# Optimization experiments

Measured on AMD Instinct MI355X. Metric: run time of the kernel, lower is better.

The kernel has to match this reference:

```python
import jax, jax.numpy as jnp
import numpy as np

B, LP, LQ, CL = 64, 64, 64, 8
VW, VC = 30002, 5002
WD, CD, CH, H, P = 300, 64, 64, 128, 20
EPS = 1e-6


def _norm(x, eps=EPS):
    # torch: sqrt(clamp(sum(x^2, -1), min=eps))
    return jnp.sqrt(jnp.maximum(jnp.sum(x * x, -1), eps))


def lstm_scan(x, Wih, Whh, b):
    # x: [N, T, D] -> outputs [N, T, Hh]; PyTorch gate order i,f,g,o
    N = x.shape[0]
    Hh = Whh.shape[1]
    xW = jnp.einsum('ntd,gd->ntg', x, Wih) + b  # precompute input projection
    def step(carry, xt):
        h, c = carry
        g = xt + h @ Whh.T
        i, f, gg, o = jnp.split(g, 4, axis=-1)
        c = jax.nn.sigmoid(f) * c + jax.nn.sigmoid(i) * jnp.tanh(gg)
        h = jax.nn.sigmoid(o) * jnp.tanh(c)
        return (h, c), h
    init = (jnp.zeros((N, Hh), x.dtype), jnp.zeros((N, Hh), x.dtype))
    _, hs = jax.lax.scan(step, init, jnp.swapaxes(xW, 0, 1))
    return jnp.swapaxes(hs, 0, 1)


def bilstm(x, Wf, Uf, bf, Wb, Ub, bb):
    fw = lstm_scan(x, Wf, Uf, bf)
    bw = jnp.flip(lstm_scan(jnp.flip(x, axis=1), Wb, Ub, bb), axis=1)
    return fw, bw


def mpm(p_fw, p_bw, q_fw, q_bw, ws):
    # ws: [8, P, H]
    def full(h1, h2, w):
        h1w = h1[:, :, None, :] * w              # [B,L,P,H]
        h2w = h2[:, -1, None, :] * w             # [B,P,H]
        num = jnp.einsum('blpd,bpd->blp', h1w, h2w)
        return num / _norm(h1w) / _norm(h2w)[:, None, :]
    def cos_matrix(x1, x2):
        num = jnp.einsum('bid,bjd->bij', x1, x2)
        return num / _norm(x1)[:, :, None] / _norm(x2)[:, None, :]
    def attentive(h1, h2, cm, w):
        h1w = h1[:, :, None, :] * w
        att = jnp.einsum('bij,bjd->bid', cm, h2) / (cm.sum(-1) + EPS)[..., None]
        attw = att[:, :, None, :] * w
        num = jnp.sum(h1w * attw, -1)
        return num / _norm(h1w) / _norm(attw)
    def max_attentive(h1, h2, cm, w):
        idx = jnp.argmax(cm, axis=-1)                           # [B,Lp]
        mv = jnp.take_along_axis(h2, idx[:, :, None], axis=1)   # [B,Lp,H]
        h1w = h1[:, :, None, :] * w
        mvw = mv[:, :, None, :] * w
        num = jnp.sum(h1w * mvw, -1)
        return num / _norm(h1w) / _norm(mvw)
    def max_pool(h1, h2, w):
        h1w = h1[:, :, None, :] * w
        h2w = h2[:, :, None, :] * w
        num = jnp.einsum('bipd,bjpd->bijp', h1w, h2w)           # [B,Lp,Lq,P]
        cos = num / _norm(h1w)[:, :, None, :] / _norm(h2w)[:, None, :, :]
        return cos.max(axis=2)
    cm_fw = cos_matrix(p_fw, q_fw)
    cm_bw = cos_matrix(p_bw, q_bw)
    return jnp.concatenate([
        full(p_fw, q_fw, ws[0]), full(p_bw, q_bw, ws[1]),
        attentive(p_fw, q_fw, cm_fw, ws[2]), attentive(p_bw, q_bw, cm_bw, ws[3]),
        max_attentive(p_fw, q_fw, cm_fw, ws[4]), max_attentive(p_bw, q_bw, cm_bw, ws[5]),
        max_pool(p_fw, q_fw, ws[6]), max_pool(p_bw, q_bw, ws[7])], axis=-1)


def setup_inputs():
    key = jax.random.key(0)
    ks = jax.random.split(key, 24)
    rn = lambda k, s, sc=0.1: jax.random.normal(k, s, dtype=jnp.float32) * sc
    def lstm_w(k, din, h):
        k1, k2 = jax.random.split(k)
        return rn(k1, (4 * h, din)), rn(k2, (4 * h, h)), jnp.zeros((4 * h,), jnp.float32)
    cWih, cWhh, cb = lstm_w(ks[4], CD, CH)
    xWf, xUf, xbf = lstm_w(ks[5], CH + WD, H)
    xWb, xUb, xbb = lstm_w(ks[6], CH + WD, H)
    aWf, aUf, abf = lstm_w(ks[7], 8 * P, H)
    aWb, aUb, abb = lstm_w(ks[8], 8 * P, H)
    return {
        'contentA_idxs': jax.random.randint(ks[0], (B, LP), 0, VW),
        'contentB_idxs': jax.random.randint(ks[1], (B, LQ), 0, VW),
        'contentA_char_idxs': jax.random.randint(ks[2], (B, LP, CL), 0, VC),
        'contentB_char_idxs': jax.random.randint(ks[3], (B, LQ, CL), 0, VC),
        'word_emb': rn(ks[9], (VW, WD), 1.0),
        'char_emb': rn(ks[10], (VC, CD), 1.0),
        'char_Wih': cWih, 'char_Whh': cWhh, 'char_b': cb,
        'ctx_Wih_f': xWf, 'ctx_Whh_f': xUf, 'ctx_b_f': xbf,
        'ctx_Wih_b': xWb, 'ctx_Whh_b': xUb, 'ctx_b_b': xbb,
        'agg_Wih_f': aWf, 'agg_Whh_f': aUf, 'agg_b_f': abf,
        'agg_Wih_b': aWb, 'agg_Whh_b': aUb, 'agg_b_b': abb,
        'mpm_w': rn(ks[11], (8, P, H), 1.0),
        'fc1_W': rn(ks[12], (2 * H, 4 * H), 0.005), 'fc1_b': jnp.zeros((2 * H,), jnp.float32),
        'fc2_W': rn(ks[13], (2, 2 * H), 0.005), 'fc2_b': jnp.zeros((2,), jnp.float32),
    }


def reference(contentA_idxs, contentB_idxs, contentA_char_idxs, contentB_char_idxs,
              word_emb, char_emb, char_Wih, char_Whh, char_b,
              ctx_Wih_f, ctx_Whh_f, ctx_b_f, ctx_Wih_b, ctx_Whh_b, ctx_b_b,
              agg_Wih_f, agg_Whh_f, agg_b_f, agg_Wih_b, agg_Whh_b, agg_b_b,
              mpm_w, fc1_W, fc1_b, fc2_W, fc2_b):
    def encode(word_idx, char_idx):
        w = word_emb[word_idx]                                   # [B,L,WD]
        L = word_idx.shape[1]
        c = char_emb[char_idx].reshape(B * L, CL, CD)
        ch = lstm_scan(c, char_Wih, char_Whh, char_b)[:, -1, :]  # last hidden
        x = jnp.concatenate([w, ch.reshape(B, L, CH)], axis=-1)
        return bilstm(x, ctx_Wih_f, ctx_Whh_f, ctx_b_f, ctx_Wih_b, ctx_Whh_b, ctx_b_b)
    p_fw, p_bw = encode(contentA_idxs, contentA_char_idxs)
    q_fw, q_bw = encode(contentB_idxs, contentB_char_idxs)
    mp = mpm(p_fw, p_bw, q_fw, q_bw, mpm_w)  # [B,LP,8P]
    mq = mpm(q_fw, q_bw, p_fw, p_bw, mpm_w)  # [B,LQ,8P]
    ap_fw, ap_bw = bilstm(mp, agg_Wih_f, agg_Whh_f, agg_b_f, agg_Wih_b, agg_Whh_b, agg_b_b)
    aq_fw, aq_bw = bilstm(mq, agg_Wih_f, agg_Whh_f, agg_b_f, agg_Wih_b, agg_Whh_b, agg_b_b)
    x = jnp.concatenate([ap_fw[:, -1], ap_bw[:, 0], aq_fw[:, -1], aq_bw[:, 0]], axis=-1)
    x = jnp.tanh(x @ fc1_W.T + fc1_b)
    return x @ fc2_W.T + fc2_b  # [B,2] logits
```

## Files before the change

kernel.cpp:

```cpp
#include <hip/hip_runtime.h>

#define EPS 1e-6f

typedef __attribute__((ext_vector_type(8))) short short8;
typedef __attribute__((ext_vector_type(8))) _Float16 half8;
typedef __attribute__((ext_vector_type(4))) float floatx4;

struct ScanArgs {
    const float* xw[4];
    const float* whh[4];
    float* out[4];
    int flipOut[4];
    int writeAll;
    int outStride;
};

struct MfArgs {
    const unsigned short* X;
    const unsigned short* W[4];
    const float* bias[4];
    float* out[4];
    int flip[4];
    int rowBase[4];
    int Kaug;
};

__device__ __forceinline__ float fsig(float x) { return 1.0f / (1.0f + __expf(-x)); }
__device__ __forceinline__ float tanh_fast(float x) {
    float e = __expf(2.f * x);
    return 1.f - 2.f / (e + 1.f);
}
__device__ __forceinline__ unsigned short f2bf(float x) {
    unsigned u = __float_as_uint(x);
    return (unsigned short)((u + 0x7fffu + ((u >> 16) & 1u)) >> 16);
}
__device__ __forceinline__ void split8_bf(const float* p, short8& hi, short8& lo) {
    #pragma unroll
    for (int e = 0; e < 8; ++e) {
        unsigned short h = f2bf(p[e]);
        float hf = __uint_as_float((unsigned)h << 16);
        hi[e] = (short)h;
        lo[e] = (short)f2bf(p[e] - hf);
    }
}
__device__ __forceinline__ void split8_f16(const float* p, half8& hi, half8& lo) {
    #pragma unroll
    for (int e = 0; e < 8; ++e) {
        _Float16 h = (_Float16)p[e];
        hi[e] = h;
        lo[e] = (_Float16)(p[e] - (float)h);
    }
}

__global__ void k_embed_word(const int* __restrict__ idxA, const int* __restrict__ idxB,
                             const float* __restrict__ emb,
                             float* __restrict__ xA, float* __restrict__ xB) {
    int row = blockIdx.x;
    const int* idx = (row < 4096) ? idxA : idxB;
    float* xout = (row < 4096) ? xA : xB;
    int r = row & 4095;
    size_t e = (size_t)idx[r];
    const float* src = emb + e * 300;
    float* dst = xout + (size_t)r * 364;
    for (int d = threadIdx.x; d < 300; d += blockDim.x) dst[d] = src[d];
}

__global__ void k_conv(const float* __restrict__ src, unsigned short* __restrict__ dst,
                       int K, int Ksec, int isW) {
    int row = blockIdx.x;
    const float* s = src + (size_t)row * K;
    unsigned short* d = dst + (size_t)row * (3 * Ksec);
    int o1 = (isW ? 2 : 1) * Ksec;
    int o2 = (isW ? 1 : 2) * Ksec;
    for (int k = threadIdx.x; k < Ksec; k += blockDim.x) {
        float x = (k < K) ? s[k] : 0.f;
        unsigned short hr = f2bf(x);
        float hif = __uint_as_float((unsigned)hr << 16);
        unsigned short lr2 = f2bf(x - hif);
        d[k]      = hr;
        d[o1 + k] = lr2;
        d[o2 + k] = hr;
    }
}

__global__ __launch_bounds__(256, 1)
void k_char_mfma(const int* __restrict__ cidxA, const int* __restrict__ cidxB,
                 const float* __restrict__ emb,
                 const unsigned short* __restrict__ WihA, const unsigned short* __restrict__ WhhA,
                 const float* __restrict__ bias,
                 float* __restrict__ xA, float* __restrict__ xB) {
    __shared__ __align__(16) float xs[32][68];
    __shared__ __align__(16) float hs[32][68];
    int tid = threadIdx.x;
    int w = tid >> 6, l = tid & 63, lr = l & 15, lc = l >> 4;
    int j = w * 16 + lr;
    short8 wih[4][6], whh[4][6];
    #pragma unroll
    for (int g = 0; g < 4; ++g)
        #pragma unroll
        for (int kt = 0; kt < 6; ++kt) {
            wih[g][kt] = *(const short8*)&WihA[(size_t)(g*64 + j)*192 + kt*32 + lc*8];
            whh[g][kt] = *(const short8*)&WhhA[(size_t)(g*64 + j)*192 + kt*32 + lc*8];
        }
    float bg[4];
    #pragma unroll
    for (int g = 0; g < 4; ++g) bg[g] = bias[g*64 + j];
    int seq0 = blockIdx.x * 32;
    for (int m = tid; m < 32*68; m += 256) (&hs[0][0])[m] = 0.f;
    float cst[2][4] = {};
    float hlast[2][4];
    __syncthreads();
    for (int t = 0; t < 8; ++t) {
        {
            int s = tid >> 3, ch = tid & 7;
            int sq = seq0 + s;
            const int* ci = (sq < 4096) ? cidxA : cidxB;
            int e = ci[(sq & 4095)*8 + t];
            float4 v0 = *(const float4*)&emb[(size_t)e*64 + ch*8];
            float4 v1 = *(const float4*)&emb[(size_t)e*64 + ch*8 + 4];
            *(float4*)&xs[s][ch*8] = v0;
            *(float4*)&xs[s][ch*8 + 4] = v1;
        }
        short8 hhi[2][2], hlo[2][2];
        if (t > 0) {
            #pragma unroll
            for (int mt = 0; mt < 2; ++mt)
                #pragma unroll
                for (int kt = 0; kt < 2; ++kt) {
                    float tmp[8];
                    *(float4*)&tmp[0] = *(const float4*)&hs[mt*16 + lr][kt*32 + lc*8];
                    *(float4*)&tmp[4] = *(const float4*)&hs[mt*16 + lr][kt*32 + lc*8 + 4];
                    split8_bf(tmp, hhi[mt][kt], hlo[mt][kt]);
                }
        }
        __syncthreads();
        short8 xhi[2][2], xlo[2][2];
        #pragma unroll
        for (int mt = 0; mt < 2; ++mt)
            #pragma unroll
            for (int kt = 0; kt < 2; ++kt) {
                float tmp[8];
                *(float4*)&tmp[0] = *(const float4*)&xs[mt*16 + lr][kt*32 + lc*8];
                *(float4*)&tmp[4] = *(const float4*)&xs[mt*16 + lr][kt*32 + lc*8 + 4];
                split8_bf(tmp, xhi[mt][kt], xlo[mt][kt]);
            }
        #pragma unroll
        for (int mt = 0; mt < 2; ++mt)
            #pragma unroll
            for (int g = 0; g < 4; ++g) {
                floatx4 a = {bg[g], bg[g], bg[g], bg[g]};
                a = __builtin_amdgcn_mfma_f32_16x16x32_bf16(xhi[mt][0], wih[g][0], a, 0, 0, 0);
                a = __builtin_amdgcn_mfma_f32_16x16x32_bf16(xhi[mt][1], wih[g][1], a, 0, 0, 0);
                a = __builtin_amdgcn_mfma_f32_16x16x32_bf16(xlo[mt][0], wih[g][2], a, 0, 0, 0);
                a = __builtin_amdgcn_mfma_f32_16x16x32_bf16(xlo[mt][1], wih[g][3], a, 0, 0, 0);
                a = __builtin_amdgcn_mfma_f32_16x16x32_bf16(xhi[mt][0], wih[g][4], a, 0, 0, 0);
                a = __builtin_amdgcn_mfma_f32_16x16x32_bf16(xhi[mt][1], wih[g][5], a, 0, 0, 0);
                if (t > 0) {
                    a = __builtin_amdgcn_mfma_f32_16x16x32_bf16(hhi[mt][0], whh[g][0], a, 0, 0, 0);
                    a = __builtin_amdgcn_mfma_f32_16x16x32_bf16(hhi[mt][1], whh[g][1], a, 0, 0, 0);
                    a = __builtin_amdgcn_mfma_f32_16x16x32_bf16(hlo[mt][0], whh[g][2], a, 0, 0, 0);
                    a = __builtin_amdgcn_mfma_f32_16x16x32_bf16(hlo[mt][1], whh[g][3], a, 0, 0, 0);
                    a = __builtin_amdgcn_mfma_f32_16x16x32_bf16(hhi[mt][0], whh[g][4], a, 0, 0, 0);
                    a = __builtin_amdgcn_mfma_f32_16x16x32_bf16(hhi[mt][1], whh[g][5], a, 0, 0, 0);
                }
                if (g == 0) { hlast[mt][0] = a[0]; hlast[mt][1] = a[1]; hlast[mt][2] = a[2]; hlast[mt][3] = a[3]; }
                else if (g == 1) {
                    #pragma unroll
                    for (int i = 0; i < 4; ++i) cst[mt][i] = fsig(a[i]) * cst[mt][i];
                } else if (g == 2) {
                    #pragma unroll
                    for (int i = 0; i < 4; ++i) cst[mt][i] += fsig(hlast[mt][i]) * tanh_fast(a[i]);
                } else {
                    #pragma unroll
                    for (int i = 0; i < 4; ++i) {
                        float h = fsig(a[i]) * tanh_fast(cst[mt][i]);
                        hlast[mt][i] = h;
                        hs[mt*16 + lc*4 + i][j] = h;
                    }
                }
            }
        __syncthreads();
    }
    #pragma unroll
    for (int mt = 0; mt < 2; ++mt)
        #pragma unroll
        for (int i = 0; i < 4; ++i) {
            int s = mt*16 + lc*4 + i;
            int sq = seq0 + s;
            float* xout = (sq < 4096) ? xA : xB;
            xout[(size_t)(sq & 4095)*364 + 300 + j] = hlast[mt][i];
        }
}

__global__ __launch_bounds__(256, 2)
void k_xw_mfma(MfArgs a) {
    int scan = blockIdx.z;
    const unsigned short* X = a.X;
    const unsigned short* W = a.W[scan];
    const float* bias = a.bias[scan];
    float* out = a.out[scan];
    int flip = a.flip[scan];
    int rowBase = a.rowBase[scan];
    int Kaug = a.Kaug;
    int m0 = blockIdx.x * 128;
    int n0 = blockIdx.y * 128;
    __shared__ __align__(16) unsigned short As[128][40];
    __shared__ __align__(16) unsigned short Bs[128][40];
    int tid = threadIdx.x;
    int wv = tid >> 6, lane = tid & 63;
    int lr = lane & 15, lc = lane >> 4;

    floatx4 acc[2][8];
    #pragma unroll
    for (int f = 0; f < 2; ++f)
        #pragma unroll
        for (int g = 0; g < 8; ++g)
            acc[f][g] = (floatx4){0.f, 0.f, 0.f, 0.f};

    int r0 = m0 + (tid >> 2);
    int r1 = r0 + 64;
    int sr0 = rowBase + (flip ? ((r0 & ~63) | (63 - (r0 & 63))) : r0);
    int sr1 = rowBase + (flip ? ((r1 & ~63) | (63 - (r1 & 63))) : r1);
    size_t asrc0 = (size_t)sr0 * Kaug + (tid & 3) * 8;
    size_t asrc1 = (size_t)sr1 * Kaug + (tid & 3) * 8;
    size_t bsrc0 = (size_t)(n0 + (tid >> 2)) * Kaug + (tid & 3) * 8;
    size_t bsrc1 = (size_t)(n0 + (tid >> 2) + 64) * Kaug + (tid & 3) * 8;
    int swrow = tid >> 2, swcol = (tid & 3) * 8;

    for (int k0 = 0; k0 < Kaug; k0 += 32) {
        short8 a0 = *(const short8*)(X + asrc0 + k0);
        short8 a1 = *(const short8*)(X + asrc1 + k0);
        short8 b0 = *(const short8*)(W + bsrc0 + k0);
        short8 b1 = *(const short8*)(W + bsrc1 + k0);
        __syncthreads();
        *(short8*)&As[swrow][swcol]      = a0;
        *(short8*)&As[swrow + 64][swcol] = a1;
        *(short8*)&Bs[swrow][swcol]      = b0;
        *(short8*)&Bs[swrow + 64][swcol] = b1;
        __syncthreads();
        short8 af0 = *(const short8*)&As[wv*32 + lr][lc*8];
        short8 af1 = *(const short8*)&As[wv*32 + 16 + lr][lc*8];
        #pragma unroll
        for (int g = 0; g < 8; ++g) {
            short8 bf = *(const short8*)&Bs[g*16 + lr][lc*8];
            acc[0][g] = __builtin_amdgcn_mfma_f32_16x16x32_bf16(af0, bf, acc[0][g], 0, 0, 0);
            acc[1][g] = __builtin_amdgcn_mfma_f32_16x16x32_bf16(af1, bf, acc[1][g], 0, 0, 0);
        }
    }

    #pragma unroll
    for (int f = 0; f < 2; ++f) {
        int row = m0 + wv*32 + f*16 + lc*4;
        #pragma unroll
        for (int g = 0; g < 8; ++g) {
            int col = n0 + g*16 + lr;
            float bv = bias[col];
            #pragma unroll
            for (int i = 0; i < 4; ++i)
                out[(size_t)(row + i)*512 + col] = acc[f][g][i] + bv;
        }
    }
}

__global__ __launch_bounds__(512, 2)
void k_lstm_scan(ScanArgs a) {
    int b = blockIdx.x;
    int scan = blockIdx.y;
    int tid = threadIdx.x;
    __shared__ __align__(16) float h_lds[128];
    __shared__ float g_lds[512];
    const float* W = a.whh[scan];
    float w[128];
    #pragma unroll
    for (int k4 = 0; k4 < 32; ++k4) {
        float4 v = *(const float4*)&W[(size_t)tid*128 + k4*4];
        w[k4*4+0]=v.x; w[k4*4+1]=v.y; w[k4*4+2]=v.z; w[k4*4+3]=v.w;
    }
    const float* xw = a.xw[scan] + (size_t)b*64*512;
    float* outp = a.out[scan];
    int flip = a.flipOut[scan];
    int wAll = a.writeAll;
    float c = 0.f;
    if (tid < 128) h_lds[tid] = 0.f;
    __syncthreads();
    for (int t = 0; t < 64; ++t) {
        float a0 = xw[t*512 + tid], a1 = 0.f, a2 = 0.f, a3 = 0.f;
        #pragma unroll
        for (int k16 = 0; k16 < 8; ++k16) {
            float4 h0 = *(const float4*)&h_lds[k16*16+0];
            float4 h1 = *(const float4*)&h_lds[k16*16+4];
            float4 h2 = *(const float4*)&h_lds[k16*16+8];
            float4 h3 = *(const float4*)&h_lds[k16*16+12];
            a0 += w[k16*16+ 0]*h0.x + w[k16*16+ 1]*h0.y + w[k16*16+ 2]*h0.z + w[k16*16+ 3]*h0.w;
            a1 += w[k16*16+ 4]*h1.x + w[k16*16+ 5]*h1.y + w[k16*16+ 6]*h1.z + w[k16*16+ 7]*h1.w;
            a2 += w[k16*16+ 8]*h2.x + w[k16*16+ 9]*h2.y + w[k16*16+10]*h2.z + w[k16*16+11]*h2.w;
            a3 += w[k16*16+12]*h3.x + w[k16*16+13]*h3.y + w[k16*16+14]*h3.z + w[k16*16+15]*h3.w;
        }
        g_lds[tid] = (a0+a1)+(a2+a3);
        __syncthreads();
        if (tid < 128) {
            float gi = g_lds[tid], gf = g_lds[128+tid], gg = g_lds[256+tid], go = g_lds[384+tid];
            c = fsig(gf)*c + fsig(gi)*tanhf(gg);
            float h = fsig(go)*tanhf(c);
            h_lds[tid] = h;
            if (wAll) {
                int tout = flip ? (63 - t) : t;
                outp[((size_t)b*64 + tout)*128 + tid] = h;
            }
        }
        __syncthreads();
    }
    if (!wAll && tid < 128)
        outp[(size_t)b * a.outStride + tid] = h_lds[tid];
}

__global__ __launch_bounds__(256, 1)
void k_cos_matrix(const float* __restrict__ pfw, const float* __restrict__ pbw,
                  const float* __restrict__ qfw, const float* __restrict__ qbw,
                  float* __restrict__ cmf, float* __restrict__ cmb) {
    int b = blockIdx.x, dir = blockIdx.y;
    const float* h1 = (dir ? pbw : pfw) + (size_t)b*8192;
    const float* h2 = (dir ? qbw : qfw) + (size_t)b*8192;
    float* cm = (dir ? cmb : cmf) + (size_t)b*4096;
    __shared__ __align__(16) float A[64][132];
    __shared__ __align__(16) float Bt[64][132];
    __shared__ float n1[64], n2[64];
    int tid = threadIdx.x;
    for (int m = tid; m < 8192; m += 256) {
        int r = m >> 7, d = m & 127;
        A[r][d] = h1[m];
        Bt[r][d] = h2[m];
    }
    __syncthreads();
    if (tid < 128) {
        const float* row = (tid < 64) ? &A[tid][0] : &Bt[tid-64][0];
        float s = 0.f;
        #pragma unroll
        for (int k4 = 0; k4 < 32; ++k4) {
            float4 v = *(const float4*)&row[k4*4];
            s += v.x*v.x + v.y*v.y + v.z*v.z + v.w*v.w;
        }
        float nv = sqrtf(fmaxf(s, EPS));
        if (tid < 64) n1[tid] = nv; else n2[tid-64] = nv;
    }
    __syncthreads();
    int tx = tid & 15, ty = tid >> 4;
    float acc[4][4] = {};
    #pragma unroll
    for (int k4 = 0; k4 < 32; ++k4) {
        float4 av[4], bv[4];
        #pragma unroll
        for (int i = 0; i < 4; ++i) av[i] = *(const float4*)&A[ty + i*16][k4*4];
        #pragma unroll
        for (int j = 0; j < 4; ++j) bv[j] = *(const float4*)&Bt[tx + j*16][k4*4];
        #pragma unroll
        for (int i = 0; i < 4; ++i)
            #pragma unroll
            for (int j = 0; j < 4; ++j)
                acc[i][j] += av[i].x*bv[j].x + av[i].y*bv[j].y + av[i].z*bv[j].z + av[i].w*bv[j].w;
    }
    #pragma unroll
    for (int i = 0; i < 4; ++i) {
        int r = ty + i*16;
        #pragma unroll
        for (int j = 0; j < 4; ++j) {
            int c2 = tx + j*16;
            cm[r*64 + c2] = acc[i][j] / (n1[r]*n2[c2]);
        }
    }
}

__global__ __launch_bounds__(512, 2)
void k_full_att(const float* __restrict__ pfw, const float* __restrict__ pbw,
                const float* __restrict__ qfw, const float* __restrict__ qbw,
                const float* __restrict__ cmf, const float* __restrict__ cmb,
                const float* __restrict__ mpmw,
                float* __restrict__ mp, float* __restrict__ mq) {
    int b = blockIdx.x, dir = blockIdx.y, which = blockIdx.z;
    const float* pd = (dir ? pbw : pfw) + (size_t)b*8192;
    const float* qd = (dir ? qbw : qfw) + (size_t)b*8192;
    const float* h1g = which ? qd : pd;
    const float* h2g = which ? pd : qd;
    const float* cmsrc = (dir ? cmb : cmf) + (size_t)b*4096;
    float* outb = which ? mq : mp;
    __shared__ __align__(16) float h2s[64][132];
    __shared__ float cms[64][68];
    __shared__ __align__(16) float wl[3*20*128];
    int tid = threadIdx.x;
    for (int m = tid; m < 8192; m += 512) {
        int r = m >> 7, d = m & 127;
        h2s[r][d] = h2g[m];
    }
    for (int m = tid; m < 4096; m += 512) {
        int l = m >> 6, j = m & 63;
        cms[l][j] = which ? cmsrc[j*64 + l] : cmsrc[m];
    }
    for (int m = tid; m < 2560; m += 512) {
        wl[m]        = mpmw[(size_t)(0+dir)*2560 + m];
        wl[2560 + m] = mpmw[(size_t)(2+dir)*2560 + m];
        wl[5120 + m] = mpmw[(size_t)(4+dir)*2560 + m];
    }
    __syncthreads();
    int l = tid >> 3, r = tid & 7;
    int d0 = r * 16;
    float h1d[16];
    #pragma unroll
    for (int q4 = 0; q4 < 4; ++q4) {
        float4 v = *(const float4*)&h1g[l*128 + d0 + q4*4];
        h1d[q4*4+0]=v.x; h1d[q4*4+1]=v.y; h1d[q4*4+2]=v.z; h1d[q4*4+3]=v.w;
    }
    float rsum = 0.f, bv = -3.4e38f; int bj = 64;
    for (int jj = 0; jj < 8; ++jj) {
        int j = r*8 + jj;
        float cv = cms[l][j];
        rsum += cv;
        if (cv > bv) { bv = cv; bj = j; }
    }
    #pragma unroll
    for (int m = 1; m < 8; m <<= 1) rsum += __shfl_xor(rsum, m, 8);
    #pragma unroll
    for (int m = 1; m < 8; m <<= 1) {
        float ov = __shfl_xor(bv, m, 8);
        int oj = __shfl_xor(bj, m, 8);
        if (ov > bv || (ov == bv && oj < bj)) { bv = ov; bj = oj; }
    }
    float att[16];
    #pragma unroll
    for (int dd = 0; dd < 16; ++dd) att[dd] = 0.f;
    for (int j = 0; j < 64; ++j) {
        float cv = cms[l][j];
        #pragma unroll
        for (int q4 = 0; q4 < 4; ++q4) {
            float4 hv = *(const float4*)&h2s[j][d0 + q4*4];
            att[q4*4+0] += cv*hv.x; att[q4*4+1] += cv*hv.y;
            att[q4*4+2] += cv*hv.z; att[q4*4+3] += cv*hv.w;
        }
    }
    float rinv = 1.f / (rsum + EPS);
    #pragma unroll
    for (int dd = 0; dd < 16; ++dd) att[dd] *= rinv;
    float mvd[16], h2l[16];
    #pragma unroll
    for (int q4 = 0; q4 < 4; ++q4) {
        float4 v = *(const float4*)&h2s[bj][d0 + q4*4];
        mvd[q4*4+0]=v.x; mvd[q4*4+1]=v.y; mvd[q4*4+2]=v.z; mvd[q4*4+3]=v.w;
        float4 u = *(const float4*)&h2s[63][d0 + q4*4];
        h2l[q4*4+0]=u.x; h2l[q4*4+1]=u.y; h2l[q4*4+2]=u.z; h2l[q4*4+3]=u.w;
    }
    size_t outrow = ((size_t)b*64 + l)*160;
    for (int pp = 0; pp < 20; ++pp) {
        const float* wf = &wl[pp*128 + d0];
        const float* wa = &wl[2560 + pp*128 + d0];
        const float* wm = &wl[5120 + pp*128 + d0];
        float fn=0,f1=0,f2=0, an=0,a1=0,a2=0, mn=0,m1=0,m2=0;
        #pragma unroll
        for (int dd = 0; dd < 16; ++dd) {
            float wfv = wf[dd], wav = wa[dd], wmv = wm[dd];
            float x1 = h1d[dd]*wfv, x2 = h2l[dd]*wfv;
            fn += x1*x2; f1 += x1*x1; f2 += x2*x2;
            float y1 = h1d[dd]*wav, y2 = att[dd]*wav;
            an += y1*y2; a1 += y1*y1; a2 += y2*y2;
            float z1 = h1d[dd]*wmv, z2 = mvd[dd]*wmv;
            mn += z1*z2; m1 += z1*z1; m2 += z2*z2;
        }
        #pragma unroll
        for (int m = 1; m < 8; m <<= 1) {
            fn += __shfl_xor(fn,m,8); f1 += __shfl_xor(f1,m,8); f2 += __shfl_xor(f2,m,8);
            an += __shfl_xor(an,m,8); a1 += __shfl_xor(a1,m,8); a2 += __shfl_xor(a2,m,8);
            mn += __shfl_xor(mn,m,8); m1 += __shfl_xor(m1,m,8); m2 += __shfl_xor(m2,m,8);
        }
        if (r == 0) {
            outb[outrow + (0+dir)*20 + pp] = fn / sqrtf(fmaxf(f1,EPS)) / sqrtf(fmaxf(f2,EPS));
            outb[outrow + (2+dir)*20 + pp] = an / sqrtf(fmaxf(a1,EPS)) / sqrtf(fmaxf(a2,EPS));
            outb[outrow + (4+dir)*20 + pp] = mn / sqrtf(fmaxf(m1,EPS)) / sqrtf(fmaxf(m2,EPS));
        }
    }
}

__global__ __launch_bounds__(256, 1)
void k_maxpool_mfma(const float* __restrict__ pfw, const float* __restrict__ pbw,
                    const float* __restrict__ qfw, const float* __restrict__ qbw,
                    const float* __restrict__ mpmw,
                    float* __restrict__ mp, float* __restrict__ mq) {
    int b = blockIdx.x, dir = blockIdx.y, pph = blockIdx.z;
    const float* h1 = (dir ? pbw : pfw) + (size_t)b*8192;
    const float* h2 = (dir ? qbw : qfw) + (size_t)b*8192;
    __shared__ __align__(16) float h1s[64][132];
    __shared__ __align__(16) float h2s[64][132];
    __shared__ __align__(16) float w2s[32][132];
    __shared__ float n1s[64][25], n2s[64][25];
    __shared__ float cpart[4][68];
    int tid = threadIdx.x;
    int w = tid >> 6, l = tid & 63, lr = l & 15, lc = l >> 4;
    for (int m = tid; m < 8192; m += 256) {
        int r = m >> 7, d = m & 127;
        h1s[r][d] = h1[m];
        h2s[r][d] = h2[m];
    }
    for (int m = tid; m < 32*128; m += 256) {
        int r = m >> 7, d = m & 127;
        float v = (r < 20) ? mpmw[(size_t)((6+dir)*20 + r)*128 + d] : 0.f;
        w2s[r][d] = v * v;
    }
    __syncthreads();
    float a1[32], b1[32];
    #pragma unroll
    for (int kt = 0; kt < 4; ++kt) {
        *(float4*)&a1[kt*8]     = *(const float4*)&h1s[w*16 + lr][kt*32 + lc*8];
        *(float4*)&a1[kt*8 + 4] = *(const float4*)&h1s[w*16 + lr][kt*32 + lc*8 + 4];
        *(float4*)&b1[kt*8]     = *(const float4*)&h2s[w*16 + lr][kt*32 + lc*8];
        *(float4*)&b1[kt*8 + 4] = *(const float4*)&h2s[w*16 + lr][kt*32 + lc*8 + 4];
    }
    half8 Bh[4][4], Bl[4][4];
    #pragma unroll
    for (int nt = 0; nt < 4; ++nt)
        #pragma unroll
        for (int kt = 0; kt < 4; ++kt) {
            float tmp[8];
            *(float4*)&tmp[0] = *(const float4*)&h2s[nt*16 + lr][kt*32 + lc*8];
            *(float4*)&tmp[4] = *(const float4*)&h2s[nt*16 + lr][kt*32 + lc*8 + 4];
            split8_f16(tmp, Bh[nt][kt], Bl[nt][kt]);
        }
    {
        float sq[32];
        half8 s1h[4], s1l[4], s2h[4], s2l[4];
        #pragma unroll
        for (int kt = 0; kt < 4; ++kt) {
            #pragma unroll
            for (int e = 0; e < 8; ++e) sq[kt*8+e] = a1[kt*8+e]*a1[kt*8+e];
            split8_f16(&sq[kt*8], s1h[kt], s1l[kt]);
        }
        #pragma unroll
        for (int kt = 0; kt < 4; ++kt) {
            #pragma unroll
            for (int e = 0; e < 8; ++e) sq[kt*8+e] = b1[kt*8+e]*b1[kt*8+e];
            split8_f16(&sq[kt*8], s2h[kt], s2l[kt]);
        }
        half8 w2h[2][4], w2l[2][4];
        #pragma unroll
        for (int nt2 = 0; nt2 < 2; ++nt2)
            #pragma unroll
            for (int kt = 0; kt < 4; ++kt) {
                float tmp[8];
                *(float4*)&tmp[0] = *(const float4*)&w2s[nt2*16 + lr][kt*32 + lc*8];
                *(float4*)&tmp[4] = *(const float4*)&w2s[nt2*16 + lr][kt*32 + lc*8 + 4];
                split8_f16(tmp, w2h[nt2][kt], w2l[nt2][kt]);
            }
        #pragma unroll
        for (int nt2 = 0; nt2 < 2; ++nt2) {
            floatx4 na1 = {0.f,0.f,0.f,0.f}, na2 = {0.f,0.f,0.f,0.f};
            #pragma unroll
            for (int kt = 0; kt < 4; ++kt) {
                na1 = __builtin_amdgcn_mfma_f32_16x16x32_f16(s1h[kt], w2h[nt2][kt], na1, 0, 0, 0);
                na2 = __builtin_amdgcn_mfma_f32_16x16x32_f16(s2h[kt], w2h[nt2][kt], na2, 0, 0, 0);
            }
            #pragma unroll
            for (int kt = 0; kt < 4; ++kt) {
                na1 = __builtin_amdgcn_mfma_f32_16x16x32_f16(s1l[kt], w2h[nt2][kt], na1, 0, 0, 0);
                na2 = __builtin_amdgcn_mfma_f32_16x16x32_f16(s2l[kt], w2h[nt2][kt], na2, 0, 0, 0);
            }
            #pragma unroll
            for (int kt = 0; kt < 4; ++kt) {
                na1 = __builtin_amdgcn_mfma_f32_16x16x32_f16(s1h[kt], w2l[nt2][kt], na1, 0, 0, 0);
                na2 = __builtin_amdgcn_mfma_f32_16x16x32_f16(s2h[kt], w2l[nt2][kt], na2, 0, 0, 0);
            }
            #pragma unroll
            for (int i = 0; i < 4; ++i) {
                int row = w*16 + lc*4 + i;
                int c2 = nt2*16 + lr;
                if (c2 < 20) {
                    n1s[row][c2] = sqrtf(fmaxf(na1[i], EPS));
                    n2s[row][c2] = sqrtf(fmaxf(na2[i], EPS));
                }
            }
        }
    }
    __syncthreads();
    for (int pi = 0; pi < 10; ++pi) {
        int pp = pph*10 + pi;
        int col = (6+dir)*20 + pp;
        half8 ah[4], al[4];
        #pragma unroll
        for (int kt = 0; kt < 4; ++kt) {
            float wv[8], aw[8];
            *(float4*)&wv[0] = *(const float4*)&w2s[pp][kt*32 + lc*8];
            *(float4*)&wv[4] = *(const float4*)&w2s[pp][kt*32 + lc*8 + 4];
            #pragma unroll
            for (int e = 0; e < 8; ++e) aw[e] = a1[kt*8+e]*wv[e];
            split8_f16(aw, ah[kt], al[kt]);
        }
        float n1v[4];
        #pragma unroll
        for (int i = 0; i < 4; ++i) n1v[i] = n1s[w*16 + lc*4 + i][pp];
        float rmax[4] = {-3.4e38f, -3.4e38f, -3.4e38f, -3.4e38f};
        float cmx[4];
        #pragma unroll
        for (int nt = 0; nt < 4; ++nt) {
            floatx4 acc = {0.f,0.f,0.f,0.f};
            #pragma unroll
            for (int kt = 0; kt < 4; ++kt)
                acc = __builtin_amdgcn_mfma_f32_16x16x32_f16(ah[kt], Bh[nt][kt], acc, 0, 0, 0);
            #pragma unroll
            for (int kt = 0; kt < 4; ++kt)
                acc = __builtin_amdgcn_mfma_f32_16x16x32_f16(al[kt], Bh[nt][kt], acc, 0, 0, 0);
            #pragma unroll
            for (int kt = 0; kt < 4; ++kt)
                acc = __builtin_amdgcn_mfma_f32_16x16x32_f16(ah[kt], Bl[nt][kt], acc, 0, 0, 0);
            float n2v = n2s[nt*16 + lr][pp];
            float cm_ = -3.4e38f;
            #pragma unroll
            for (int i = 0; i < 4; ++i) {
                float cv = acc[i] / (n1v[i] * n2v);
                rmax[i] = fmaxf(rmax[i], cv);
                cm_ = fmaxf(cm_, cv);
            }
            cmx[nt] = cm_;
        }
        #pragma unroll
        for (int msk = 1; msk < 16; msk <<= 1)
            #pragma unroll
            for (int i = 0; i < 4; ++i) rmax[i] = fmaxf(rmax[i], __shfl_xor(rmax[i], msk));
        if (lr == 0) {
            #pragma unroll
            for (int i = 0; i < 4; ++i)
                mp[((size_t)b*64 + w*16 + lc*4 + i)*160 + col] = rmax[i];
        }
        #pragma unroll
        for (int msk = 16; msk < 64; msk <<= 1)
            #pragma unroll
            for (int nt = 0; nt < 4; ++nt) cmx[nt] = fmaxf(cmx[nt], __shfl_xor(cmx[nt], msk));
        if (lc == 0) {
            #pragma unroll
            for (int nt = 0; nt < 4; ++nt) cpart[w][nt*16 + lr] = cmx[nt];
        }
        __syncthreads();
        if (tid < 64) {
            float mv = fmaxf(fmaxf(cpart[0][tid], cpart[1][tid]),
                             fmaxf(cpart[2][tid], cpart[3][tid]));
            mq[((size_t)b*64 + tid)*160 + col] = mv;
        }
        __syncthreads();
    }
}

__global__ void k_fc(const float* __restrict__ xcat,
                     const float* __restrict__ fc1W, const float* __restrict__ fc1b,
                     const float* __restrict__ fc2W, const float* __restrict__ fc2b,
                     float* __restrict__ out) {
    int b = blockIdx.x;
    int tid = threadIdx.x;
    __shared__ float y[256];
    const float* x = xcat + (size_t)b*512;
    float acc = fc1b[tid];
    #pragma unroll 8
    for (int k4 = 0; k4 < 128; ++k4) {
        float4 wv = *(const float4*)&fc1W[(size_t)tid*512 + k4*4];
        float4 xv = *(const float4*)&x[k4*4];
        acc += wv.x*xv.x + wv.y*xv.y + wv.z*xv.z + wv.w*xv.w;
    }
    y[tid] = tanhf(acc);
    __syncthreads();
    if (tid < 2) {
        float o = fc2b[tid];
        for (int k = 0; k < 256; ++k) o += y[k]*fc2W[tid*256 + k];
        out[b*2 + tid] = o;
    }
}

extern "C" void kernel_launch(void* const* d_in, const int* in_sizes, int n_in,
                              void* d_out, int out_size, void* d_ws, size_t ws_size,
                              hipStream_t stream) {
    (void)in_sizes; (void)n_in; (void)out_size; (void)ws_size;
    const int* idxA  = (const int*)d_in[0];
    const int* idxB  = (const int*)d_in[1];
    const int* cidxA = (const int*)d_in[2];
    const int* cidxB = (const int*)d_in[3];
    const float* wemb = (const float*)d_in[4];
    const float* cemb = (const float*)d_in[5];
    const float* cWih = (const float*)d_in[6];
    const float* cWhh = (const float*)d_in[7];
    const float* cb   = (const float*)d_in[8];
    const float* xWf = (const float*)d_in[9];
    const float* xUf = (const float*)d_in[10];
    const float* xbf = (const float*)d_in[11];
    const float* xWb = (const float*)d_in[12];
    const float* xUb = (const float*)d_in[13];
    const float* xbb = (const float*)d_in[14];
    const float* aWf = (const float*)d_in[15];
    const float* aUf = (const float*)d_in[16];
    const float* abf = (const float*)d_in[17];
    const float* aWb = (const float*)d_in[18];
    const float* aUb = (const float*)d_in[19];
    const float* abb = (const float*)d_in[20];
    const float* mpmw = (const float*)d_in[21];
    const float* fc1W = (const float*)d_in[22];
    const float* fc1b = (const float*)d_in[23];
    const float* fc2W = (const float*)d_in[24];
    const float* fc2b = (const float*)d_in[25];
    float* out = (float*)d_out;

    float* ws = (float*)d_ws;
    float* xA  = ws; ws += (size_t)4096*364;
    float* xB  = ws; ws += (size_t)4096*364;
    float* xw0 = ws; ws += (size_t)4096*512;
    float* xw1 = ws; ws += (size_t)4096*512;
    float* xw2 = ws; ws += (size_t)4096*512;
    float* xw3 = ws; ws += (size_t)4096*512;
    float* pfw = ws; ws += (size_t)4096*128;
    float* pbw = ws; ws += (size_t)4096*128;
    float* qfw = ws; ws += (size_t)4096*128;
    float* qbw = ws; ws += (size_t)4096*128;
    float* cmf = ws; ws += (size_t)64*64*64;
    float* cmb = ws; ws += (size_t)64*64*64;
    float* mp  = ws; ws += (size_t)4096*160;
    float* mq  = ws; ws += (size_t)4096*160;
    float* xcat = ws; ws += (size_t)64*512;
    unsigned short* Xaug = (unsigned short*)ws; ws += (size_t)8192*1152/2;
    unsigned short* Wfa  = (unsigned short*)ws; ws += (size_t)512*1152/2;
    unsigned short* Wba  = (unsigned short*)ws; ws += (size_t)512*1152/2;
    unsigned short* WihC = (unsigned short*)ws; ws += (size_t)256*192/2;
    unsigned short* WhhC = (unsigned short*)ws; ws += (size_t)256*192/2;

    k_conv<<<256, 128, 0, stream>>>(cWih, WihC, 64, 64, 1);
    k_conv<<<256, 128, 0, stream>>>(cWhh, WhhC, 64, 64, 1);
    k_embed_word<<<8192, 128, 0, stream>>>(idxA, idxB, wemb, xA, xB);
    k_char_mfma<<<256, 256, 0, stream>>>(cidxA, cidxB, cemb, WihC, WhhC, cb, xA, xB);
    k_conv<<<4096, 128, 0, stream>>>(xA, Xaug, 364, 384, 0);
    k_conv<<<4096, 128, 0, stream>>>(xB, Xaug + (size_t)4096*1152, 364, 384, 0);
    k_conv<<<512, 128, 0, stream>>>(xWf, Wfa, 364, 384, 1);
    k_conv<<<512, 128, 0, stream>>>(xWb, Wba, 364, 384, 1);
    MfArgs cx;
    cx.X = Xaug;
    cx.W[0]=Wfa; cx.W[1]=Wfa; cx.W[2]=Wba; cx.W[3]=Wba;
    cx.bias[0]=xbf; cx.bias[1]=xbf; cx.bias[2]=xbb; cx.bias[3]=xbb;
    cx.out[0]=xw0; cx.out[1]=xw1; cx.out[2]=xw2; cx.out[3]=xw3;
    cx.flip[0]=0; cx.flip[1]=0; cx.flip[2]=1; cx.flip[3]=1;
    cx.rowBase[0]=0; cx.rowBase[1]=4096; cx.rowBase[2]=0; cx.rowBase[3]=4096;
    cx.Kaug = 1152;
    k_xw_mfma<<<dim3(32, 4, 4), 256, 0, stream>>>(cx);
    ScanArgs cs;
    cs.xw[0]=xw0; cs.xw[1]=xw1; cs.xw[2]=xw2; cs.xw[3]=xw3;
    cs.whh[0]=xUf; cs.whh[1]=xUf; cs.whh[2]=xUb; cs.whh[3]=xUb;
    cs.out[0]=pfw; cs.out[1]=qfw; cs.out[2]=pbw; cs.out[3]=qbw;
    cs.flipOut[0]=0; cs.flipOut[1]=0; cs.flipOut[2]=1; cs.flipOut[3]=1;
    cs.writeAll = 1; cs.outStride = 0;
    k_lstm_scan<<<dim3(64, 4), 512, 0, stream>>>(cs);
    k_cos_matrix<<<dim3(64, 2), 256, 0, stream>>>(pfw, pbw, qfw, qbw, cmf, cmb);
    k_full_att<<<dim3(64, 2, 2), 512, 0, stream>>>(pfw, pbw, qfw, qbw, cmf, cmb, mpmw, mp, mq);
    k_maxpool_mfma<<<dim3(64, 2, 2), 256, 0, stream>>>(pfw, pbw, qfw, qbw, mpmw, mp, mq);
    k_conv<<<4096, 128, 0, stream>>>(mp, Xaug, 160, 160, 0);
    k_conv<<<4096, 128, 0, stream>>>(mq, Xaug + (size_t)4096*480, 160, 160, 0);
    k_conv<<<512, 128, 0, stream>>>(aWf, Wfa, 160, 160, 1);
    k_conv<<<512, 128, 0, stream>>>(aWb, Wba, 160, 160, 1);
    MfArgs ax;
    ax.X = Xaug;
    ax.W[0]=Wfa; ax.W[1]=Wfa; ax.W[2]=Wba; ax.W[3]=Wba;
    ax.bias[0]=abf; ax.bias[1]=abf; ax.bias[2]=abb; ax.bias[3]=abb;
    ax.out[0]=xw0; ax.out[1]=xw1; ax.out[2]=xw2; ax.out[3]=xw3;
    ax.flip[0]=0; ax.flip[1]=0; ax.flip[2]=1; ax.flip[3]=1;
    ax.rowBase[0]=0; ax.rowBase[1]=4096; ax.rowBase[2]=0; ax.rowBase[3]=4096;
    ax.Kaug = 480;
    k_xw_mfma<<<dim3(32, 4, 4), 256, 0, stream>>>(ax);
    ScanArgs as;
    as.xw[0]=xw0; as.xw[1]=xw1; as.xw[2]=xw2; as.xw[3]=xw3;
    as.whh[0]=aUf; as.whh[1]=aUf; as.whh[2]=aUb; as.whh[3]=aUb;
    as.out[0]=xcat+0; as.out[1]=xcat+256; as.out[2]=xcat+128; as.out[3]=xcat+384;
    as.flipOut[0]=0; as.flipOut[1]=0; as.flipOut[2]=0; as.flipOut[3]=0;
    as.writeAll = 0; as.outStride = 512;
    k_lstm_scan<<<dim3(64, 4), 512, 0, stream>>>(as);
    k_fc<<<64, 256, 0, stream>>>(xcat, fc1W, fc1b, fc2W, fc2b, out);
}
```

Baseline: 416.7 us.

## Run LSTM recurrence on MFMA with split-bf16 weights, batching sequences per block

Replaces the per-sequence fp32 scalar recurrent scan with an MFMA kernel that processes 16 sequences per block. The recurrent weights and the hidden state are each split into bf16 hi and lo parts, and three MFMA products approximate fp32 precision. Gate columns are permuted in the xW projection output and in the packed weights, so each wave holds all four gates for its hidden units in registers and the cell update runs without an LDS gate exchange. The grid shrinks from 256 blocks to 16, which trades parallelism across the GPU for denser matrix throughput on each sequential step. It also adds four small weight-packing launches.

```diff
diff --git a/kernel.cpp b/kernel.cpp
--- a/kernel.cpp
+++ b/kernel.cpp
@@ -6,9 +6,9 @@
 typedef __attribute__((ext_vector_type(8))) _Float16 half8;
 typedef __attribute__((ext_vector_type(4))) float floatx4;
 
-struct ScanArgs {
+struct Scan2Args {
     const float* xw[4];
-    const float* whh[4];
+    const unsigned short* whhp[4];
     float* out[4];
     int flipOut[4];
     int writeAll;
@@ -80,6 +80,21 @@
         d[k]      = hr;
         d[o1 + k] = lr2;
         d[o2 + k] = hr;
+    }
+}
+
+__global__ void k_conv_whh(const float* __restrict__ W, unsigned short* __restrict__ dst) {
+    int r = blockIdx.x;
+    int gate = r >> 7, j = r & 127;
+    int rp = ((j >> 4) << 6) + gate*16 + (j & 15);
+    const float* s = W + (size_t)r * 128;
+    unsigned short* d = dst + (size_t)rp * 256;
+    for (int k = threadIdx.x; k < 128; k += blockDim.x) {
+        float x = s[k];
+        unsigned short h = f2bf(x);
+        float hf = __uint_as_float((unsigned)h << 16);
+        d[k] = h;
+        d[128 + k] = f2bf(x - hf);
     }
 }
 
@@ -254,64 +269,102 @@
         #pragma unroll
         for (int g = 0; g < 8; ++g) {
             int col = n0 + g*16 + lr;
+            int jj = col & 127, gate = col >> 7;
+            int colp = ((jj >> 4) << 6) + gate*16 + (jj & 15);
             float bv = bias[col];
             #pragma unroll
             for (int i = 0; i < 4; ++i)
-                out[(size_t)(row + i)*512 + col] = acc[f][g][i] + bv;
-        }
-    }
-}
-
-__global__ __launch_bounds__(512, 2)
-void k_lstm_scan(ScanArgs a) {
-    int b = blockIdx.x;
+                out[(size_t)(row + i)*512 + colp] = acc[f][g][i] + bv;
+        }
+    }
+}
+
+__global__ __launch_bounds__(512)
+void k_lstm_mfma(Scan2Args a) {
+    int bg = blockIdx.x;
     int scan = blockIdx.y;
     int tid = threadIdx.x;
-    __shared__ __align__(16) float h_lds[128];
-    __shared__ float g_lds[512];
-    const float* W = a.whh[scan];
-    float w[128];
-    #pragma unroll
-    for (int k4 = 0; k4 < 32; ++k4) {
-        float4 v = *(const float4*)&W[(size_t)tid*128 + k4*4];
-        w[k4*4+0]=v.x; w[k4*4+1]=v.y; w[k4*4+2]=v.z; w[k4*4+3]=v.w;
-    }
-    const float* xw = a.xw[scan] + (size_t)b*64*512;
+    int w = tid >> 6, l = tid & 63, lr = l & 15, lc = l >> 4;
+    __shared__ __align__(16) unsigned short hs_hi[16][136];
+    __shared__ __align__(16) unsigned short hs_lo[16][136];
+    const unsigned short* Wp = a.whhp[scan];
+    short8 Bhi[4][4], Blo[4][4];
+    #pragma unroll
+    for (int nt = 0; nt < 4; ++nt)
+        #pragma unroll
+        for (int kt = 0; kt < 4; ++kt) {
+            int row = w*64 + nt*16 + lr;
+            Bhi[nt][kt] = *(const short8*)&Wp[(size_t)row*256 + kt*32 + lc*8];
+            Blo[nt][kt] = *(const short8*)&Wp[(size_t)row*256 + 128 + kt*32 + lc*8];
+        }
+    const float* xw = a.xw[scan];
     float* outp = a.out[scan];
     int flip = a.flipOut[scan];
     int wAll = a.writeAll;
-    float c = 0.f;
-    if (tid < 128) h_lds[tid] = 0.f;
+    int bloc = lc * 4;
+    int j = w*16 + lr;
+    float cst[4] = {0.f, 0.f, 0.f, 0.f};
+    for (int m = tid; m < 16*136; m += 512) {
+        (&hs_hi[0][0])[m] = 0;
+        (&hs_lo[0][0])[m] = 0;
+    }
     __syncthreads();
     for (int t = 0; t < 64; ++t) {
-        float a0 = xw[t*512 + tid], a1 = 0.f, a2 = 0.f, a3 = 0.f;
-        #pragma unroll
-        for (int k16 = 0; k16 < 8; ++k16) {
-            float4 h0 = *(const float4*)&h_lds[k16*16+0];
-            float4 h1 = *(const float4*)&h_lds[k16*16+4];
-            float4 h2 = *(const float4*)&h_lds[k16*16+8];
-            float4 h3 = *(const float4*)&h_lds[k16*16+12];
-            a0 += w[k16*16+ 0]*h0.x + w[k16*16+ 1]*h0.y + w[k16*16+ 2]*h0.z + w[k16*16+ 3]*h0.w;
-            a1 += w[k16*16+ 4]*h1.x + w[k16*16+ 5]*h1.y + w[k16*16+ 6]*h1.z + w[k16*16+ 7]*h1.w;
-            a2 += w[k16*16+ 8]*h2.x + w[k16*16+ 9]*h2.y + w[k16*16+10]*h2.z + w[k16*16+11]*h2.w;
-            a3 += w[k16*16+12]*h3.x + w[k16*16+13]*h3.y + w[k16*16+14]*h3.z + w[k16*16+15]*h3.w;
-        }
-        g_lds[tid] = (a0+a1)+(a2+a3);
+        float xwv[4][4];
+        #pragma unroll
+        for (int nt = 0; nt < 4; ++nt)
+            #pragma unroll
+            for (int i = 0; i < 4; ++i) {
+                int bglob = bg*16 + bloc + i;
+                xwv[nt][i] = xw[((size_t)bglob*64 + t)*512 + w*64 + nt*16 + lr];
+            }
+        floatx4 acc[4];
+        #pragma unroll
+        for (int nt = 0; nt < 4; ++nt) acc[nt] = (floatx4){0.f, 0.f, 0.f, 0.f};
+        if (t > 0) {
+            short8 Ahi[4], Alo[4];
+            #pragma unroll
+            for (int kt = 0; kt < 4; ++kt) {
+                Ahi[kt] = *(const short8*)&hs_hi[lr][kt*32 + lc*8];
+                Alo[kt] = *(const short8*)&hs_lo[lr][kt*32 + lc*8];
+            }
+            #pragma unroll
+            for (int nt = 0; nt < 4; ++nt) {
+                #pragma unroll
+                for (int kt = 0; kt < 4; ++kt)
+                    acc[nt] = __builtin_amdgcn_mfma_f32_16x16x32_bf16(Ahi[kt], Bhi[nt][kt], acc[nt], 0, 0, 0);
+                #pragma unroll
+                for (int kt = 0; kt < 4; ++kt)
+                    acc[nt] = __builtin_amdgcn_mfma_f32_16x16x32_bf16(Alo[kt], Bhi[nt][kt], acc[nt], 0, 0, 0);
+                #pragma unroll
+                for (int kt = 0; kt < 4; ++kt)
+                    acc[nt] = __builtin_amdgcn_mfma_f32_16x16x32_bf16(Ahi[kt], Blo[nt][kt], acc[nt], 0, 0, 0);
+            }
+        }
         __syncthreads();
-        if (tid < 128) {
-            float gi = g_lds[tid], gf = g_lds[128+tid], gg = g_lds[256+tid], go = g_lds[384+tid];
-            c = fsig(gf)*c + fsig(gi)*tanhf(gg);
-            float h = fsig(go)*tanhf(c);
-            h_lds[tid] = h;
+        #pragma unroll
+        for (int i = 0; i < 4; ++i) {
+            float gi = acc[0][i] + xwv[0][i];
+            float gf = acc[1][i] + xwv[1][i];
+            float gg = acc[2][i] + xwv[2][i];
+            float go = acc[3][i] + xwv[3][i];
+            float c = fsig(gf)*cst[i] + fsig(gi)*tanh_fast(gg);
+            cst[i] = c;
+            float h = fsig(go)*tanh_fast(c);
+            unsigned short hh = f2bf(h);
+            float hf = __uint_as_float((unsigned)hh << 16);
+            unsigned short hl = f2bf(h - hf);
+            hs_hi[bloc + i][j] = hh;
+            hs_lo[bloc + i][j] = hl;
             if (wAll) {
                 int tout = flip ? (63 - t) : t;
-                outp[((size_t)b*64 + tout)*128 + tid] = h;
+                outp[(((size_t)(bg*16 + bloc + i))*64 + tout)*128 + j] = h;
+            } else if (t == 63) {
+                outp[(size_t)(bg*16 + bloc + i) * a.outStride + j] = h;
             }
         }
         __syncthreads();
     }
-    if (!wAll && tid < 128)
-        outp[(size_t)b * a.outStride + tid] = h_lds[tid];
 }
 
 __global__ __launch_bounds__(256, 1)
@@ -720,9 +773,17 @@
     unsigned short* Wba  = (unsigned short*)ws; ws += (size_t)512*1152/2;
     unsigned short* WihC = (unsigned short*)ws; ws += (size_t)256*192/2;
     unsigned short* WhhC = (unsigned short*)ws; ws += (size_t)256*192/2;
+    unsigned short* UfP  = (unsigned short*)ws; ws += (size_t)512*256/2;
+    unsigned short* UbP  = (unsigned short*)ws; ws += (size_t)512*256/2;
+    unsigned short* AfP  = (unsigned short*)ws; ws += (size_t)512*256/2;
+    unsigned short* AbP  = (unsigned short*)ws; ws += (size_t)512*256/2;
 
     k_conv<<<256, 128, 0, stream>>>(cWih, WihC, 64, 64, 1);
     k_conv<<<256, 128, 0, stream>>>(cWhh, WhhC, 64, 64, 1);
+    k_conv_whh<<<512, 128, 0, stream>>>(xUf, UfP);
+    k_conv_whh<<<512, 128, 0, stream>>>(xUb, UbP);
+    k_conv_whh<<<512, 128, 0, stream>>>(aUf, AfP);
+    k_conv_whh<<<512, 128, 0, stream>>>(aUb, AbP);
     k_embed_word<<<8192, 128, 0, stream>>>(idxA, idxB, wemb, xA, xB);
     k_char_mfma<<<256, 256, 0, stream>>>(cidxA, cidxB, cemb, WihC, WhhC, cb, xA, xB);
     k_conv<<<4096, 128, 0, stream>>>(xA, Xaug, 364, 384, 0);
@@ -738,13 +799,13 @@
     cx.rowBase[0]=0; cx.rowBase[1]=4096; cx.rowBase[2]=0; cx.rowBase[3]=4096;
     cx.Kaug = 1152;
     k_xw_mfma<<<dim3(32, 4, 4), 256, 0, stream>>>(cx);
-    ScanArgs cs;
+    Scan2Args cs;
     cs.xw[0]=xw0; cs.xw[1]=xw1; cs.xw[2]=xw2; cs.xw[3]=xw3;
-    cs.whh[0]=xUf; cs.whh[1]=xUf; cs.whh[2]=xUb; cs.whh[3]=xUb;
+    cs.whhp[0]=UfP; cs.whhp[1]=UfP; cs.whhp[2]=UbP; cs.whhp[3]=UbP;
     cs.out[0]=pfw; cs.out[1]=qfw; cs.out[2]=pbw; cs.out[3]=qbw;
     cs.flipOut[0]=0; cs.flipOut[1]=0; cs.flipOut[2]=1; cs.flipOut[3]=1;
     cs.writeAll = 1; cs.outStride = 0;
-    k_lstm_scan<<<dim3(64, 4), 512, 0, stream>>>(cs);
+    k_lstm_mfma<<<dim3(4, 4), 512, 0, stream>>>(cs);
     k_cos_matrix<<<dim3(64, 2), 256, 0, stream>>>(pfw, pbw, qfw, qbw, cmf, cmb);
     k_full_att<<<dim3(64, 2, 2), 512, 0, stream>>>(pfw, pbw, qfw, qbw, cmf, cmb, mpmw, mp, mq);
     k_maxpool_mfma<<<dim3(64, 2, 2), 256, 0, stream>>>(pfw, pbw, qfw, qbw, mpmw, mp, mq);
@@ -761,12 +822,12 @@
     ax.rowBase[0]=0; ax.rowBase[1]=4096; ax.rowBase[2]=0; ax.rowBase[3]=4096;
     ax.Kaug = 480;
     k_xw_mfma<<<dim3(32, 4, 4), 256, 0, stream>>>(ax);
-    ScanArgs as;
+    Scan2Args as;
     as.xw[0]=xw0; as.xw[1]=xw1; as.xw[2]=xw2; as.xw[3]=xw3;
-    as.whh[0]=aUf; as.whh[1]=aUf; as.whh[2]=aUb; as.whh[3]=aUb;
+    as.whhp[0]=AfP; as.whhp[1]=AfP; as.whhp[2]=AbP; as.whhp[3]=AbP;
     as.out[0]=xcat+0; as.out[1]=xcat+256; as.out[2]=xcat+128; as.out[3]=xcat+384;
     as.flipOut[0]=0; as.flipOut[1]=0; as.flipOut[2]=0; as.flipOut[3]=0;
     as.writeAll = 0; as.outStride = 512;
-    k_lstm_scan<<<dim3(64, 4), 512, 0, stream>>>(as);
+    k_lstm_mfma<<<dim3(4, 4), 512, 0, stream>>>(as);
     k_fc<<<64, 256, 0, stream>>>(xcat, fc1W, fc1b, fc2W, fc2b, out);
 }
```

Measured after the change: 539.8 us. 1.3x slower.
